# Kernel tuning notes

Hardware: AMD Instinct MI355X
Metric: run time of the kernel (lower is better)

The kernel has to match this reference:

```python
import jax, jax.numpy as jnp
import numpy as np

HIDDEN = 2048
INTER = 5632
B, S = 2, 2048


def _ternary(key, shape):
    # values in {-1, 0, +1}, matching 2-bit packed ternary weights
    return jax.random.randint(key, shape, -1, 2).astype(jnp.float32)


def setup_inputs() -> dict:
    key = jax.random.key(0)
    ks = jax.random.split(key, 7)
    x = jax.random.normal(ks[0], (B, S, HIDDEN), dtype=jnp.float32)
    gate_w = _ternary(ks[1], (INTER, HIDDEN))   # [intermediate, hidden]
    up_w = _ternary(ks[2], (INTER, HIDDEN))     # [intermediate, hidden]
    down_w = _ternary(ks[3], (HIDDEN, INTER))   # [hidden, intermediate]
    # per-output-channel dequant scales (positive, as from absmean quantization)
    gate_s = jax.random.uniform(ks[4], (INTER,), minval=0.01, maxval=0.1, dtype=jnp.float32)
    up_s = jax.random.uniform(ks[5], (INTER,), minval=0.01, maxval=0.1, dtype=jnp.float32)
    down_s = jax.random.uniform(ks[6], (HIDDEN,), minval=0.01, maxval=0.1, dtype=jnp.float32)
    return {"x": x, "gate_w": gate_w, "up_w": up_w, "down_w": down_w,
            "gate_s": gate_s, "up_s": up_s, "down_s": down_s}


def reference(x, gate_w, up_w, down_w, gate_s, up_s, down_s):
    # x: (B, S, H) -> flatten tokens, as in forward_hidden
    b, s, h = x.shape
    xf = x.reshape(b * s, h)
    # ternary linear = add/sub-only matmul + per-channel scale
    g = jnp.einsum('th,ih->ti', xf, gate_w) * gate_s   # (T, I)
    u = jnp.einsum('th,ih->ti', xf, up_w) * up_s       # (T, I)
    hdn = jax.nn.silu(g) * u                            # gated activation
    out = jnp.einsum('ti,hi->th', hdn, down_w) * down_s  # (T, H)
    return out.reshape(b, s, -1)
```

## Files before the change

kernel.cpp:

```cpp
#include <hip/hip_runtime.h>
#include <stdint.h>
#include <stddef.h>

#define HIDDEN 2048
#define INTER  5632
#define TOKENS 4096
#define BK     32
#define BKI    64

typedef __attribute__((ext_vector_type(8))) _Float16 f16x8;
typedef __attribute__((ext_vector_type(4))) _Float16 f16x4;
typedef __attribute__((ext_vector_type(4))) float    f32x4;
typedef __attribute__((ext_vector_type(4))) int      i32x4;

__global__ __launch_bounds__(256)
void quant_x(const float* __restrict__ x, int8_t* __restrict__ xq,
             float* __restrict__ xs) {
    const int t   = blockIdx.x;
    const int tid = threadIdx.x;
    const float4* row = (const float4*)(x + (size_t)t * HIDDEN);
    float4 v0 = row[tid * 2];
    float4 v1 = row[tid * 2 + 1];
    float m = fmaxf(fmaxf(fabsf(v0.x), fabsf(v0.y)), fmaxf(fabsf(v0.z), fabsf(v0.w)));
    m = fmaxf(m, fmaxf(fmaxf(fabsf(v1.x), fabsf(v1.y)), fmaxf(fabsf(v1.z), fabsf(v1.w))));
    #pragma unroll
    for (int off = 32; off; off >>= 1)
        m = fmaxf(m, __shfl_xor(m, off, 64));
    __shared__ float wmax[4];
    if ((tid & 63) == 0) wmax[tid >> 6] = m;
    __syncthreads();
    m = fmaxf(fmaxf(wmax[0], wmax[1]), fmaxf(wmax[2], wmax[3]));
    m = fmaxf(m, 1e-20f);
    if (tid == 0) xs[t] = m * (1.0f / 127.0f);
    const float inv = 127.0f / m;
    float vals[8] = {v0.x, v0.y, v0.z, v0.w, v1.x, v1.y, v1.z, v1.w};
    int b[8];
    #pragma unroll
    for (int i = 0; i < 8; ++i) b[i] = (int)rintf(vals[i] * inv);
    int lo = (b[0] & 255) | ((b[1] & 255) << 8) | ((b[2] & 255) << 16) | (b[3] << 24);
    int hi = (b[4] & 255) | ((b[5] & 255) << 8) | ((b[6] & 255) << 16) | (b[7] << 24);
    ((int2*)(xq + (size_t)t * HIDDEN))[tid] = make_int2(lo, hi);
}

__global__ void cvt_w(const float4* __restrict__ gw, const float4* __restrict__ uw,
                      const float4* __restrict__ dw,
                      int* __restrict__ go, int* __restrict__ uo,
                      f16x4* __restrict__ dno) {
    const int NW4 = INTER * HIDDEN / 4;
    int i = blockIdx.x * blockDim.x + threadIdx.x;
    const int stride = gridDim.x * blockDim.x;
    for (; i < 3 * NW4; i += stride) {
        if (i < 2 * NW4) {
            const bool is_g = i < NW4;
            const int j = is_g ? i : i - NW4;
            float4 f = is_g ? gw[j] : uw[j];
            int p = ((int)(signed char)(int)f.x & 255)
                  | (((int)(signed char)(int)f.y & 255) << 8)
                  | (((int)(signed char)(int)f.z & 255) << 16)
                  | (((int)(signed char)(int)f.w) << 24);
            if (is_g) go[j] = p; else uo[j] = p;
        } else {
            const int j = i - 2 * NW4;
            float4 f = dw[j];
            f16x4 o;
            o.x = (_Float16)f.x; o.y = (_Float16)f.y;
            o.z = (_Float16)f.z; o.w = (_Float16)f.w;
            dno[j] = o;
        }
    }
}

__global__ __launch_bounds__(256, 2)
void gemm_gateup(const int8_t* __restrict__ Xq,
                 const int8_t* __restrict__ Wg,
                 const int8_t* __restrict__ Wu,
                 const float* __restrict__ xs,
                 const float* __restrict__ gs,
                 const float* __restrict__ us,
                 _Float16* __restrict__ Hm) {
    __shared__ int8_t As [128 * BKI];
    __shared__ int8_t Bgs[128 * BKI];
    __shared__ int8_t Bus[128 * BKI];

    const int tid  = threadIdx.x;
    const int lane = tid & 63;
    const int wave = tid >> 6;
    const int wm   = (wave >> 1) * 64;
    const int wn   = (wave & 1) * 64;
    const int bm   = blockIdx.y * 128;
    const int bn   = blockIdx.x * 128;
    const int l15  = lane & 15;
    const int lq   = lane >> 4;

    const int f0 = tid,       f1 = tid + 256;
    const int row0 = f0 >> 2, row1 = f1 >> 2;
    const int sg0 = (f0 & 3) * 16, sg1 = (f1 & 3) * 16;

    const int8_t* gX0 = Xq + (size_t)(bm + row0) * HIDDEN + sg0;
    const int8_t* gX1 = Xq + (size_t)(bm + row1) * HIDDEN + sg1;
    const int8_t* gG0 = Wg + (size_t)(bn + row0) * HIDDEN + sg0;
    const int8_t* gG1 = Wg + (size_t)(bn + row1) * HIDDEN + sg1;
    const int8_t* gU0 = Wu + (size_t)(bn + row0) * HIDDEN + sg0;
    const int8_t* gU1 = Wu + (size_t)(bn + row1) * HIDDEN + sg1;

    i32x4 accg[4][4] = {};
    i32x4 accu[4][4] = {};

    for (int k0 = 0; k0 < HIDDEN; k0 += BKI) {
        __builtin_amdgcn_global_load_lds(
            (__attribute__((address_space(1))) void*)(gX0 + k0),
            (__attribute__((address_space(3))) void*)&As[f0 * 16], 16, 0, 0);
        __builtin_amdgcn_global_load_lds(
            (__attribute__((address_space(1))) void*)(gX1 + k0),
            (__attribute__((address_space(3))) void*)&As[f1 * 16], 16, 0, 0);
        __builtin_amdgcn_global_load_lds(
            (__attribute__((address_space(1))) void*)(gG0 + k0),
            (__attribute__((address_space(3))) void*)&Bgs[f0 * 16], 16, 0, 0);
        __builtin_amdgcn_global_load_lds(
            (__attribute__((address_space(1))) void*)(gG1 + k0),
            (__attribute__((address_space(3))) void*)&Bgs[f1 * 16], 16, 0, 0);
        __builtin_amdgcn_global_load_lds(
            (__attribute__((address_space(1))) void*)(gU0 + k0),
            (__attribute__((address_space(3))) void*)&Bus[f0 * 16], 16, 0, 0);
        __builtin_amdgcn_global_load_lds(
            (__attribute__((address_space(1))) void*)(gU1 + k0),
            (__attribute__((address_space(3))) void*)&Bus[f1 * 16], 16, 0, 0);
        __syncthreads();

        i32x4 a[4];
        #pragma unroll
        for (int im = 0; im < 4; ++im)
            a[im] = *(const i32x4*)&As[(wm + im * 16 + l15) * BKI + lq * 16];
        #pragma unroll
        for (int jn = 0; jn < 4; ++jn) {
            i32x4 bg = *(const i32x4*)&Bgs[(wn + jn * 16 + l15) * BKI + lq * 16];
            i32x4 bu = *(const i32x4*)&Bus[(wn + jn * 16 + l15) * BKI + lq * 16];
            #pragma unroll
            for (int im = 0; im < 4; ++im) {
                accg[im][jn] = __builtin_amdgcn_mfma_i32_16x16x64_i8(a[im], bg, accg[im][jn], 0, 0, 0);
                accu[im][jn] = __builtin_amdgcn_mfma_i32_16x16x64_i8(a[im], bu, accu[im][jn], 0, 0, 0);
            }
        }
        __syncthreads();
    }

    #pragma unroll
    for (int jn = 0; jn < 4; ++jn) {
        const int col = bn + wn + jn * 16 + l15;
        const float sg = gs[col];
        const float su = us[col];
        #pragma unroll
        for (int im = 0; im < 4; ++im) {
            const int rbase = bm + wm + im * 16 + lq * 4;
            #pragma unroll
            for (int r = 0; r < 4; ++r) {
                const int row = rbase + r;
                const float st = xs[row];
                float g = (float)accg[im][jn][r] * st * sg;
                float u = (float)accu[im][jn][r] * st * su;
                float h = (g / (1.0f + __expf(-g))) * u;
                Hm[(size_t)row * INTER + col] = (_Float16)h;
            }
        }
    }
}

__global__ __launch_bounds__(256, 2)
void gemm_down(const _Float16* __restrict__ Hm,
               const _Float16* __restrict__ Wd,
               const float* __restrict__ dsc,
               float* __restrict__ out) {
    __shared__ _Float16 As[128 * BK];
    __shared__ _Float16 Bs[128 * BK];

    const int tid  = threadIdx.x;
    const int lane = tid & 63;
    const int wave = tid >> 6;
    const int wm   = (wave >> 1) * 64;
    const int wn   = (wave & 1) * 64;
    const int bm   = blockIdx.y * 128;
    const int bn   = blockIdx.x * 128;
    const int l15  = lane & 15;
    const int lq   = lane >> 4;

    const int f0 = tid,       f1 = tid + 256;
    const int row0 = f0 >> 2, row1 = f1 >> 2;
    const int sg0 = (f0 & 3) * 8, sg1 = (f1 & 3) * 8;

    const _Float16* gA0 = Hm + (size_t)(bm + row0) * INTER + sg0;
    const _Float16* gA1 = Hm + (size_t)(bm + row1) * INTER + sg1;
    const _Float16* gB0 = Wd + (size_t)(bn + row0) * INTER + sg0;
    const _Float16* gB1 = Wd + (size_t)(bn + row1) * INTER + sg1;

    f32x4 acc[4][4] = {};

    for (int k0 = 0; k0 < INTER; k0 += BK) {
        __builtin_amdgcn_global_load_lds(
            (__attribute__((address_space(1))) void*)(gA0 + k0),
            (__attribute__((address_space(3))) void*)&As[f0 * 8], 16, 0, 0);
        __builtin_amdgcn_global_load_lds(
            (__attribute__((address_space(1))) void*)(gA1 + k0),
            (__attribute__((address_space(3))) void*)&As[f1 * 8], 16, 0, 0);
        __builtin_amdgcn_global_load_lds(
            (__attribute__((address_space(1))) void*)(gB0 + k0),
            (__attribute__((address_space(3))) void*)&Bs[f0 * 8], 16, 0, 0);
        __builtin_amdgcn_global_load_lds(
            (__attribute__((address_space(1))) void*)(gB1 + k0),
            (__attribute__((address_space(3))) void*)&Bs[f1 * 8], 16, 0, 0);
        __syncthreads();

        f16x8 a[4];
        #pragma unroll
        for (int im = 0; im < 4; ++im)
            a[im] = *(const f16x8*)&As[(wm + im * 16 + l15) * BK + lq * 8];
        #pragma unroll
        for (int jn = 0; jn < 4; ++jn) {
            f16x8 b = *(const f16x8*)&Bs[(wn + jn * 16 + l15) * BK + lq * 8];
            #pragma unroll
            for (int im = 0; im < 4; ++im)
                acc[im][jn] = __builtin_amdgcn_mfma_f32_16x16x32_f16(a[im], b, acc[im][jn], 0, 0, 0);
        }
        __syncthreads();
    }

    #pragma unroll
    for (int jn = 0; jn < 4; ++jn) {
        const int col = bn + wn + jn * 16 + l15;
        const float sd = dsc[col];
        #pragma unroll
        for (int im = 0; im < 4; ++im) {
            const int rbase = bm + wm + im * 16 + lq * 4;
            #pragma unroll
            for (int r = 0; r < 4; ++r)
                out[(size_t)(rbase + r) * HIDDEN + col] = acc[im][jn][r] * sd;
        }
    }
}

extern "C" void kernel_launch(void* const* d_in, const int* in_sizes, int n_in,
                              void* d_out, int out_size, void* d_ws, size_t ws_size,
                              hipStream_t stream) {
    const float* x   = (const float*)d_in[0];
    const float* gw  = (const float*)d_in[1];
    const float* uw  = (const float*)d_in[2];
    const float* dw  = (const float*)d_in[3];
    const float* gsc = (const float*)d_in[4];
    const float* usc = (const float*)d_in[5];
    const float* dsc = (const float*)d_in[6];
    float* out = (float*)d_out;

    char* ws = (char*)d_ws;
    int8_t*   Xq  = (int8_t*)(ws);
    int8_t*   Wg8 = (int8_t*)(ws + 8388608ull);
    int8_t*   Wu8 = (int8_t*)(ws + 19922944ull);
    _Float16* Wdh = (_Float16*)(ws + 31457280ull);
    _Float16* Hm  = (_Float16*)(ws + 54525952ull);
    float*    xs  = (float*)(ws + 100663296ull);

    quant_x<<<TOKENS, 256, 0, stream>>>(x, Xq, xs);
    cvt_w<<<2048, 256, 0, stream>>>((const float4*)gw, (const float4*)uw,
                                    (const float4*)dw,
                                    (int*)Wg8, (int*)Wu8, (f16x4*)Wdh);

    gemm_gateup<<<dim3(INTER / 128, TOKENS / 128), 256, 0, stream>>>(
        Xq, Wg8, Wu8, xs, gsc, usc, Hm);
    gemm_down<<<dim3(HIDDEN / 128, TOKENS / 128), 256, 0, stream>>>(
        Hm, Wdh, dsc, out);
}
```

Before: 418.8 us.

## Split-K the down GEMM, swizzle tile order, add fp16 partial reduction

The down-projection GEMM is split into two K halves to double the block count (256 to 512 tiles) and occupancy is raised to 4 blocks per SM. The fp16 partial sums are combined and scaled in a new reduce kernel. Both GEMMs now use a 1D grid with grouped tile ordering so neighbouring blocks share A/B tiles in L2. The cost is an extra kernel, extra partial-buffer traffic, and reduced precision from storing the partials as fp16. The workspace layout is reshuffled so the partial buffer reuses the Xq/weight region.

```diff
diff --git a/kernel.cpp b/kernel.cpp
--- a/kernel.cpp
+++ b/kernel.cpp
@@ -82,13 +82,16 @@
     __shared__ int8_t Bgs[128 * BKI];
     __shared__ int8_t Bus[128 * BKI];
 
+    const int pid   = blockIdx.x;
+    const int local = pid % (16 * 44);
+    const int bm    = ((pid / (16 * 44)) * 16 + (local & 15)) * 128;
+    const int bn    = (local >> 4) * 128;
+
     const int tid  = threadIdx.x;
     const int lane = tid & 63;
     const int wave = tid >> 6;
     const int wm   = (wave >> 1) * 64;
     const int wn   = (wave & 1) * 64;
-    const int bm   = blockIdx.y * 128;
-    const int bn   = blockIdx.x * 128;
     const int l15  = lane & 15;
     const int lq   = lane >> 4;
 
@@ -165,21 +168,26 @@
     }
 }
 
-__global__ __launch_bounds__(256, 2)
+__global__ __launch_bounds__(256, 4)
 void gemm_down(const _Float16* __restrict__ Hm,
                const _Float16* __restrict__ Wd,
-               const float* __restrict__ dsc,
-               float* __restrict__ out) {
+               _Float16* __restrict__ part) {
     __shared__ _Float16 As[128 * BK];
     __shared__ _Float16 Bs[128 * BK];
+
+    const int pid = blockIdx.x;
+    const int seg = pid >> 9;
+    const int s   = pid & 511;
+    const int loc = s & 255;
+    const int bm  = ((s >> 8) * 16 + (loc & 15)) * 128;
+    const int bn  = (loc >> 4) * 128;
+    const int kbeg = seg * (INTER / 2);
 
     const int tid  = threadIdx.x;
     const int lane = tid & 63;
     const int wave = tid >> 6;
     const int wm   = (wave >> 1) * 64;
     const int wn   = (wave & 1) * 64;
-    const int bm   = blockIdx.y * 128;
-    const int bn   = blockIdx.x * 128;
     const int l15  = lane & 15;
     const int lq   = lane >> 4;
 
@@ -187,14 +195,14 @@
     const int row0 = f0 >> 2, row1 = f1 >> 2;
     const int sg0 = (f0 & 3) * 8, sg1 = (f1 & 3) * 8;
 
-    const _Float16* gA0 = Hm + (size_t)(bm + row0) * INTER + sg0;
-    const _Float16* gA1 = Hm + (size_t)(bm + row1) * INTER + sg1;
-    const _Float16* gB0 = Wd + (size_t)(bn + row0) * INTER + sg0;
-    const _Float16* gB1 = Wd + (size_t)(bn + row1) * INTER + sg1;
+    const _Float16* gA0 = Hm + (size_t)(bm + row0) * INTER + kbeg + sg0;
+    const _Float16* gA1 = Hm + (size_t)(bm + row1) * INTER + kbeg + sg1;
+    const _Float16* gB0 = Wd + (size_t)(bn + row0) * INTER + kbeg + sg0;
+    const _Float16* gB1 = Wd + (size_t)(bn + row1) * INTER + kbeg + sg1;
 
     f32x4 acc[4][4] = {};
 
-    for (int k0 = 0; k0 < INTER; k0 += BK) {
+    for (int k0 = 0; k0 < INTER / 2; k0 += BK) {
         __builtin_amdgcn_global_load_lds(
             (__attribute__((address_space(1))) void*)(gA0 + k0),
             (__attribute__((address_space(3))) void*)&As[f0 * 8], 16, 0, 0);
@@ -223,17 +231,36 @@
         __syncthreads();
     }
 
+    _Float16* po = part + (size_t)seg * TOKENS * HIDDEN;
     #pragma unroll
     for (int jn = 0; jn < 4; ++jn) {
         const int col = bn + wn + jn * 16 + l15;
-        const float sd = dsc[col];
         #pragma unroll
         for (int im = 0; im < 4; ++im) {
             const int rbase = bm + wm + im * 16 + lq * 4;
             #pragma unroll
             for (int r = 0; r < 4; ++r)
-                out[(size_t)(rbase + r) * HIDDEN + col] = acc[im][jn][r] * sd;
-        }
+                po[(size_t)(rbase + r) * HIDDEN + col] = (_Float16)acc[im][jn][r];
+        }
+    }
+}
+
+__global__ void reduce_down(const f16x4* __restrict__ p,
+                            const float* __restrict__ dsc,
+                            float4* __restrict__ out) {
+    const int N4 = TOKENS * HIDDEN / 4;
+    int i = blockIdx.x * blockDim.x + threadIdx.x;
+    const int stride = gridDim.x * blockDim.x;
+    for (; i < N4; i += stride) {
+        f16x4 a = p[i];
+        f16x4 b = p[i + N4];
+        const int c = (i * 4) & (HIDDEN - 1);
+        float4 o;
+        o.x = ((float)a.x + (float)b.x) * dsc[c];
+        o.y = ((float)a.y + (float)b.y) * dsc[c + 1];
+        o.z = ((float)a.z + (float)b.z) * dsc[c + 2];
+        o.w = ((float)a.w + (float)b.w) * dsc[c + 3];
+        out[i] = o;
     }
 }
 
@@ -250,20 +277,22 @@
     float* out = (float*)d_out;
 
     char* ws = (char*)d_ws;
-    int8_t*   Xq  = (int8_t*)(ws);
-    int8_t*   Wg8 = (int8_t*)(ws + 8388608ull);
-    int8_t*   Wu8 = (int8_t*)(ws + 19922944ull);
-    _Float16* Wdh = (_Float16*)(ws + 31457280ull);
-    _Float16* Hm  = (_Float16*)(ws + 54525952ull);
-    float*    xs  = (float*)(ws + 100663296ull);
+    _Float16* Wdh  = (_Float16*)(ws);
+    _Float16* Hm   = (_Float16*)(ws + 23068672ull);
+    int8_t*   Xq   = (int8_t*)(ws + 69206016ull);
+    int8_t*   Wg8  = (int8_t*)(ws + 77594624ull);
+    int8_t*   Wu8  = (int8_t*)(ws + 89128960ull);
+    _Float16* part = (_Float16*)(ws + 69206016ull);
+    float*    xs   = (float*)(ws + 102760448ull);
 
     quant_x<<<TOKENS, 256, 0, stream>>>(x, Xq, xs);
     cvt_w<<<2048, 256, 0, stream>>>((const float4*)gw, (const float4*)uw,
                                     (const float4*)dw,
                                     (int*)Wg8, (int*)Wu8, (f16x4*)Wdh);
 
-    gemm_gateup<<<dim3(INTER / 128, TOKENS / 128), 256, 0, stream>>>(
+    gemm_gateup<<<(INTER / 128) * (TOKENS / 128), 256, 0, stream>>>(
         Xq, Wg8, Wu8, xs, gsc, usc, Hm);
-    gemm_down<<<dim3(HIDDEN / 128, TOKENS / 128), 256, 0, stream>>>(
-        Hm, Wdh, dsc, out);
-}
+    gemm_down<<<2 * (HIDDEN / 128) * (TOKENS / 128), 256, 0, stream>>>(
+        Hm, Wdh, part);
+    reduce_down<<<2048, 256, 0, stream>>>((const f16x4*)part, dsc, (float4*)out);
+}
```

New measurement: 435.3 us. 1.04x slower.

## Swizzle LDS tiles to avoid bank conflicts and group-order GEMM blocks for L2 reuse

Applied to the files above, without the earlier changes.

Both GEMM kernels now store each 16-byte chunk of a row at a rotated position in LDS, chosen by the row index, and read it back through the matching swizzle. This is meant to spread the MFMA operand reads across LDS banks. The grids are also flattened to 1D and remapped so that groups of 16 row tiles sweep the column tiles together, which should improve L2 reuse of the weight and activation tiles. The swizzle adds some integer address arithmetic, and the mapping must cover every tile exactly once.

```diff
diff --git a/kernel.cpp b/kernel.cpp
--- a/kernel.cpp
+++ b/kernel.cpp
@@ -12,6 +12,10 @@
 typedef __attribute__((ext_vector_type(4))) _Float16 f16x4;
 typedef __attribute__((ext_vector_type(4))) float    f32x4;
 typedef __attribute__((ext_vector_type(4))) int      i32x4;
+
+__device__ __forceinline__ int swz_slot(int row, int q) {
+    return row * 4 + ((q + (row >> 1)) & 3);
+}
 
 __global__ __launch_bounds__(256)
 void quant_x(const float* __restrict__ x, int8_t* __restrict__ xq,
@@ -82,19 +86,23 @@
     __shared__ int8_t Bgs[128 * BKI];
     __shared__ int8_t Bus[128 * BKI];
 
+    const int pid   = blockIdx.x;
+    const int local = pid % (16 * 44);
+    const int bm    = ((pid / (16 * 44)) * 16 + (local & 15)) * 128;
+    const int bn    = (local >> 4) * 128;
+
     const int tid  = threadIdx.x;
     const int lane = tid & 63;
     const int wave = tid >> 6;
     const int wm   = (wave >> 1) * 64;
     const int wn   = (wave & 1) * 64;
-    const int bm   = blockIdx.y * 128;
-    const int bn   = blockIdx.x * 128;
     const int l15  = lane & 15;
     const int lq   = lane >> 4;
 
     const int f0 = tid,       f1 = tid + 256;
     const int row0 = f0 >> 2, row1 = f1 >> 2;
-    const int sg0 = (f0 & 3) * 16, sg1 = (f1 & 3) * 16;
+    const int sg0 = (((f0 & 3) - (row0 >> 1)) & 3) * 16;
+    const int sg1 = (((f1 & 3) - (row1 >> 1)) & 3) * 16;
 
     const int8_t* gX0 = Xq + (size_t)(bm + row0) * HIDDEN + sg0;
     const int8_t* gX1 = Xq + (size_t)(bm + row1) * HIDDEN + sg1;
@@ -129,12 +137,15 @@
 
         i32x4 a[4];
         #pragma unroll
-        for (int im = 0; im < 4; ++im)
-            a[im] = *(const i32x4*)&As[(wm + im * 16 + l15) * BKI + lq * 16];
+        for (int im = 0; im < 4; ++im) {
+            const int r = wm + im * 16 + l15;
+            a[im] = *(const i32x4*)&As[swz_slot(r, lq) * 16];
+        }
         #pragma unroll
         for (int jn = 0; jn < 4; ++jn) {
-            i32x4 bg = *(const i32x4*)&Bgs[(wn + jn * 16 + l15) * BKI + lq * 16];
-            i32x4 bu = *(const i32x4*)&Bus[(wn + jn * 16 + l15) * BKI + lq * 16];
+            const int r = wn + jn * 16 + l15;
+            i32x4 bg = *(const i32x4*)&Bgs[swz_slot(r, lq) * 16];
+            i32x4 bu = *(const i32x4*)&Bus[swz_slot(r, lq) * 16];
             #pragma unroll
             for (int im = 0; im < 4; ++im) {
                 accg[im][jn] = __builtin_amdgcn_mfma_i32_16x16x64_i8(a[im], bg, accg[im][jn], 0, 0, 0);
@@ -173,19 +184,23 @@
     __shared__ _Float16 As[128 * BK];
     __shared__ _Float16 Bs[128 * BK];
 
+    const int pid = blockIdx.x;
+    const int loc = pid & 255;
+    const int bm  = ((pid >> 8) * 16 + (loc & 15)) * 128;
+    const int bn  = (loc >> 4) * 128;
+
     const int tid  = threadIdx.x;
     const int lane = tid & 63;
     const int wave = tid >> 6;
     const int wm   = (wave >> 1) * 64;
     const int wn   = (wave & 1) * 64;
-    const int bm   = blockIdx.y * 128;
-    const int bn   = blockIdx.x * 128;
     const int l15  = lane & 15;
     const int lq   = lane >> 4;
 
     const int f0 = tid,       f1 = tid + 256;
     const int row0 = f0 >> 2, row1 = f1 >> 2;
-    const int sg0 = (f0 & 3) * 8, sg1 = (f1 & 3) * 8;
+    const int sg0 = (((f0 & 3) - (row0 >> 1)) & 3) * 8;
+    const int sg1 = (((f1 & 3) - (row1 >> 1)) & 3) * 8;
 
     const _Float16* gA0 = Hm + (size_t)(bm + row0) * INTER + sg0;
     const _Float16* gA1 = Hm + (size_t)(bm + row1) * INTER + sg1;
@@ -211,11 +226,14 @@
 
         f16x8 a[4];
         #pragma unroll
-        for (int im = 0; im < 4; ++im)
-            a[im] = *(const f16x8*)&As[(wm + im * 16 + l15) * BK + lq * 8];
+        for (int im = 0; im < 4; ++im) {
+            const int r = wm + im * 16 + l15;
+            a[im] = *(const f16x8*)&As[swz_slot(r, lq) * 8];
+        }
         #pragma unroll
         for (int jn = 0; jn < 4; ++jn) {
-            f16x8 b = *(const f16x8*)&Bs[(wn + jn * 16 + l15) * BK + lq * 8];
+            const int r = wn + jn * 16 + l15;
+            f16x8 b = *(const f16x8*)&Bs[swz_slot(r, lq) * 8];
             #pragma unroll
             for (int im = 0; im < 4; ++im)
                 acc[im][jn] = __builtin_amdgcn_mfma_f32_16x16x32_f16(a[im], b, acc[im][jn], 0, 0, 0);
@@ -262,8 +280,8 @@
                                     (const float4*)dw,
                                     (int*)Wg8, (int*)Wu8, (f16x4*)Wdh);
 
-    gemm_gateup<<<dim3(INTER / 128, TOKENS / 128), 256, 0, stream>>>(
+    gemm_gateup<<<(INTER / 128) * (TOKENS / 128), 256, 0, stream>>>(
         Xq, Wg8, Wu8, xs, gsc, usc, Hm);
-    gemm_down<<<dim3(HIDDEN / 128, TOKENS / 128), 256, 0, stream>>>(
+    gemm_down<<<(HIDDEN / 128) * (TOKENS / 128), 256, 0, stream>>>(
         Hm, Wdh, dsc, out);
 }
```

Result: no change. 417.3 us (-0.4%).
